# Kernel tuning notes

Measured on AMD Instinct MI355X. Metric: run time of the kernel, lower is better.

## Reference

```python
import jax, jax.numpy as jnp
import numpy as np

N = 50000          # num_assets / nodes
E = 1_600_000      # edges (avg degree 32)
F = 128            # num_features
R = 4              # num_relations
H = 1              # heads
O1, O2 = 15, 10    # RGATConv out_channels (hard-coded in module)
NEG_SLOPE = 0.2    # leaky_relu slope in RGATConv
BN_EPS = 1e-5


def setup_inputs() -> dict:
    key = jax.random.key(0)
    ks = jax.random.split(key, 24)
    s = 0.1
    return {
        "node_emb": jax.random.normal(ks[0], (N, F), jnp.float32),
        "edge_index": jax.random.randint(ks[1], (2, E), 0, N),
        "edge_types": jax.random.randint(ks[2], (E,), 0, R),
        "edge_attr": jax.random.normal(ks[3], (E, 1), jnp.float32),
        # RGATConv layer 1 params
        "W1": jax.random.normal(ks[4], (R, F, H * O1), jnp.float32) * s,
        "q1": jax.random.normal(ks[5], (H * O1, H), jnp.float32) * s,
        "k1": jax.random.normal(ks[6], (H * O1, H), jnp.float32) * s,
        "e1": jax.random.normal(ks[7], (H * O1, H), jnp.float32) * s,
        "We1": jax.random.normal(ks[8], (1, H * O1), jnp.float32) * s,  # lin_edge
        "b1": jax.random.normal(ks[9], (H * O1,), jnp.float32) * s,
        # RGATConv layer 2 params
        "W2": jax.random.normal(ks[10], (R, H * O1, H * O2), jnp.float32) * s,
        "q2": jax.random.normal(ks[11], (H * O2, H), jnp.float32) * s,
        "k2": jax.random.normal(ks[12], (H * O2, H), jnp.float32) * s,
        "e2": jax.random.normal(ks[13], (H * O2, H), jnp.float32) * s,
        "We2": jax.random.normal(ks[14], (1, H * O2), jnp.float32) * s,
        "b2": jax.random.normal(ks[15], (O2,), jnp.float32) * s,
        # BatchNorm affine params
        "g1": 1.0 + jax.random.normal(ks[16], (H * O1,), jnp.float32) * 0.05,
        "beta1": jax.random.normal(ks[17], (H * O1,), jnp.float32) * 0.05,
        "g2": 1.0 + jax.random.normal(ks[18], (O2,), jnp.float32) * 0.05,
        "beta2": jax.random.normal(ks[19], (O2,), jnp.float32) * 0.05,
        # head Linear(10, 1)
        "w_head": jax.random.normal(ks[20], (O2, 1), jnp.float32) * s,
        "b_head": jax.random.normal(ks[21], (1,), jnp.float32) * s,
    }


def _segment_softmax(alpha, dst, n):
    amax = jax.ops.segment_max(alpha, dst, num_segments=n)
    ex = jnp.exp(alpha - amax[dst])
    denom = jax.ops.segment_sum(ex, dst, num_segments=n)
    return ex / (denom[dst] + 1e-16)


def _rgat(x, src, dst, etype, eattr, W, q, k, e, We, b, heads, out_ch, concat):
    n = x.shape[0]
    # per-relation transform of all nodes, then gather per-edge (same math as
    # PyG's per-edge bmm with W[edge_type])
    xt = jnp.einsum('nf,rfo->nro', x, W)            # [N, R, H*O]
    out_i = xt[dst, etype]                          # [E, H*O] (target)
    out_j = xt[src, etype]                          # [E, H*O] (source)
    alpha = out_i @ q + out_j @ k + (eattr @ We) @ e  # [E, H]
    alpha = jax.nn.leaky_relu(alpha, NEG_SLOPE)
    alpha = _segment_softmax(alpha, dst, n)          # across-relation softmax over dst
    msg = (alpha[:, :, None] * out_j.reshape(-1, heads, out_ch)).reshape(-1, heads * out_ch)
    agg = jax.ops.segment_sum(msg, dst, num_segments=n)
    if not concat:
        agg = agg.reshape(n, heads, out_ch).mean(axis=1)
    return agg + b


def _bn_elu(x, g, beta):
    # training-mode BatchNorm1d (batch statistics, biased variance) + ELU
    mu = x.mean(axis=0)
    var = x.var(axis=0)
    xh = (x - mu) / jnp.sqrt(var + BN_EPS)
    return jax.nn.elu(xh * g + beta)


def reference(node_emb, edge_index, edge_types, edge_attr,
              W1, q1, k1, e1, We1, b1,
              W2, q2, k2, e2, We2, b2,
              g1, beta1, g2, beta2, w_head, b_head):
    src, dst = edge_index[0], edge_index[1]
    x = _rgat(node_emb, src, dst, edge_types, edge_attr,
              W1, q1, k1, e1, We1, b1, H, O1, True)
    x = _bn_elu(x, g1, beta1)
    x = _rgat(x, src, dst, edge_types, edge_attr,
              W2, q2, k2, e2, We2, b2, H, O2, False)
    x = _bn_elu(x, g2, beta2)
    return x @ w_head + b_head                       # [N, 1]
```

## Files before the change

kernel.cpp:

```cpp
#include <hip/hip_runtime.h>


typedef unsigned short ushort_t;
typedef unsigned int uint_t;
typedef __attribute__((ext_vector_type(8))) short bf16x8;
typedef __attribute__((ext_vector_type(4))) float f32x4;

#define NEG_SLOPE 0.2f
#define BN_EPS 1e-5f
#define NBUCK 512

__device__ __forceinline__ float bf2f(ushort_t u) {
    return __uint_as_float(((uint_t)u) << 16);
}
__device__ __forceinline__ ushort_t f2bf(float f) {
    uint_t x = __float_as_uint(f);
    x += 0x7FFFu + ((x >> 16) & 1u);
    return (ushort_t)(x >> 16);
}
__device__ __forceinline__ float h2f(ushort_t u) {
    _Float16 h = __builtin_bit_cast(_Float16, u);
    return (float)h;
}
__device__ __forceinline__ ushort_t f2h(float f) {
    _Float16 h = (_Float16)f;
    return __builtin_bit_cast(ushort_t, h);
}
__device__ __forceinline__ float loadf(const void* p, int i, int isb) {
    return isb ? bf2f(((const ushort_t*)p)[i]) : ((const float*)p)[i];
}
__device__ __forceinline__ float sel4(float a0, float a1, float a2, float a3, int et) {
    float lo = (et == 1) ? a1 : a0;
    float hi = (et == 3) ? a3 : a2;
    return (et >= 2) ? hi : lo;
}

__global__ __launch_bounds__(256) void k_prep(const uint_t* __restrict__ x,
                                              const void* __restrict__ W1,
                                              const void* __restrict__ W2,
                                              const void* __restrict__ q1b,
                                              const void* __restrict__ k1b,
                                              const void* __restrict__ We1,
                                              const void* __restrict__ e1v,
                                              const void* __restrict__ We2,
                                              const void* __restrict__ e2v,
                                              int* __restrict__ dflag,
                                              int* __restrict__ bcur,
                                              float* __restrict__ stats1,
                                              float* __restrict__ stats2,
                                              float* __restrict__ cbuf,
                                              ushort_t* __restrict__ Wsw,
                                              float* __restrict__ Wf2, int cap) {
    __shared__ int cnt;
    int t = threadIdx.x;
    if (t == 0) cnt = 0;
    __syncthreads();
    uint_t u = x[t * 37];
    uint_t lo_exp = (u >> 7) & 0xFF;
    atomicAdd(&cnt, (lo_exp >= 96 && lo_exp <= 150) ? 1 : 0);
    __syncthreads();
    int isb = (cnt > 192) ? 1 : 0;
    if (blockIdx.x == 0) {
        if (t == 0) {
            dflag[0] = isb;
            float c1 = 0.f;
            for (int o = 0; o < 15; ++o) c1 += loadf(We1, o, isb) * loadf(e1v, o, isb);
            float c2 = 0.f;
            for (int o = 0; o < 10; ++o) c2 += loadf(We2, o, isb) * loadf(e2v, o, isb);
            cbuf[0] = c1;
            cbuf[1] = c2;
        }
        for (int i = t; i < NBUCK; i += 256) bcur[i] = i * cap;
        stats1[t] = 0.f;
        stats2[t] = 0.f;
        for (int idx = t; idx < 15 * 40; idx += 256) {
            int f = idx / 40, j = idx % 40, r = j / 10, o = j % 10;
            Wf2[idx] = loadf(W2, (r * 15 + f) * 10 + o, isb);
        }
    }
    for (int idx = blockIdx.x * 256 + t; idx < 20 * 64 * 8; idx += gridDim.x * 256) {
        int j = idx & 7, lane = (idx >> 3) & 63, fr = idx >> 9;
        int ks = fr / 5, ct = fr % 5;
        int k = ks * 32 + (lane >> 4) * 8 + j;
        int c = ct * 16 + (lane & 15);
        float v = 0.f;
        if (c < 64) {
            int r = c >> 4, o = c & 15;
            if (o < 15) {
                v = loadf(W1, (r * 128 + k) * 15 + o, isb);
            } else {
                float s = 0.f;
#pragma unroll
                for (int oo = 0; oo < 15; ++oo)
                    s += loadf(W1, (r * 128 + k) * 15 + oo, isb) * loadf(k1b, oo, isb);
                v = s;
            }
        } else if (c < 68) {
            int r = c - 64;
            float s = 0.f;
#pragma unroll
            for (int oo = 0; oo < 15; ++oo)
                s += loadf(W1, (r * 128 + k) * 15 + oo, isb) * loadf(q1b, oo, isb);
            v = s;
        }
        Wsw[idx] = f2bf(v);
    }
}

__global__ __launch_bounds__(512) void k_bucket(const int* __restrict__ ei,
                                                const int* __restrict__ et,
                                                const void* __restrict__ ea,
                                                const int* __restrict__ flag,
                                                int* __restrict__ bcur,
                                                int2* __restrict__ tmp,
                                                int E, int npb) {
    extern __shared__ int2 srec[];
    __shared__ int cnt[NBUCK];
    __shared__ int lofs[NBUCK + 1];
    __shared__ int gpos[NBUCK];
    int t = threadIdx.x;
    int isb = flag[0];
    cnt[t] = 0;
    __syncthreads();
    int e0 = blockIdx.x * 8192;
    for (int i = 0; i < 16; ++i) {
        int e = e0 + i * 512 + t;
        if (e < E) atomicAdd(&cnt[ei[E + e] / npb], 1);
    }
    __syncthreads();
    int myc = cnt[t];
    for (int off = 1; off < NBUCK; off <<= 1) {
        int v = (t >= off) ? cnt[t - off] : 0;
        __syncthreads();
        cnt[t] += v;
        __syncthreads();
    }
    lofs[t] = cnt[t] - myc;
    if (t == NBUCK - 1) lofs[NBUCK] = cnt[NBUCK - 1];
    __syncthreads();
    cnt[t] = lofs[t];
    __syncthreads();
    for (int i = 0; i < 16; ++i) {
        int e = e0 + i * 512 + t;
        if (e < E) {
            int d = ei[E + e];
            int b = d / npb;
            int ldst = d - b * npb;
            int idx = atomicAdd(&cnt[b], 1);
            int2 r;
            r.x = (int)((uint_t)ei[e] | ((uint_t)et[e] << 23) | ((uint_t)ldst << 25));
            r.y = __float_as_int(loadf(ea, e, isb));
            srec[idx] = r;
        }
    }
    __syncthreads();
    int c_b = lofs[t + 1] - lofs[t];
    gpos[t] = atomicAdd(&bcur[t], c_b);
    __syncthreads();
    int total = lofs[NBUCK];
    for (int i = t; i < total; i += 512) {
        int lo = 0, hi = NBUCK - 1;
        while (lo < hi) {
            int mid = (lo + hi + 1) >> 1;
            if (lofs[mid] <= i) lo = mid; else hi = mid - 1;
        }
        tmp[gpos[lo] + (i - lofs[lo])] = srec[i];
    }
}

__global__ __launch_bounds__(256) void k_b2csr(const int2* __restrict__ tmp,
                                               const int* __restrict__ bcur,
                                               int* __restrict__ rs,
                                               int* __restrict__ re,
                                               int2* __restrict__ ebuf,
                                               int N, int npb, int cap) {
    __shared__ int cnt[128];
    __shared__ int lofs[129];
    int b = blockIdx.x, t = threadIdx.x;
    int s0 = b * cap;
    int s1 = bcur[b];
    if (t < 128) cnt[t] = 0;
    __syncthreads();
    for (int p = s0 + t; p < s1; p += 256) {
        uint_t x = (uint_t)tmp[p].x;
        atomicAdd(&cnt[(x >> 25) & 0x7F], 1);
    }
    __syncthreads();
    int myc = (t < 128) ? cnt[t] : 0;
    for (int off = 1; off < 128; off <<= 1) {
        int v = (t >= off && t < 128) ? cnt[t - off] : 0;
        __syncthreads();
        if (t < 128) cnt[t] += v;
        __syncthreads();
    }
    if (t < 128) {
        lofs[t] = cnt[t] - myc;
        if (t == 127) lofs[128] = cnt[127];
    }
    __syncthreads();
    int node0 = b * npb;
    if (t < npb && node0 + t < N) {
        rs[node0 + t] = s0 + lofs[t];
        re[node0 + t] = s0 + lofs[t + 1];
    }
    if (t < 128) cnt[t] = lofs[t];
    __syncthreads();
    for (int p = s0 + t; p < s1; p += 256) {
        int2 r = tmp[p];
        uint_t x = (uint_t)r.x;
        int ldst = (x >> 25) & 0x7F;
        int idx = atomicAdd(&cnt[ldst], 1);
        int2 o;
        o.x = (int)(x & 0x7FFFFF) | (((int)(x >> 23) & 3) << 20);
        o.y = (int)(((uint_t)(node0 + ldst) << 16) |
                    (uint_t)f2bf(__int_as_float(r.y)));
        ebuf[s0 + idx] = o;
    }
}

__global__ __launch_bounds__(256) void k_t1(const void* __restrict__ xin,
                                            const ushort_t* __restrict__ Wsw,
                                            const int* __restrict__ flag,
                                            ushort_t* __restrict__ xt,
                                            float* __restrict__ dq,
                                            int N, int ntiles, int nwaves) {
    int isb = flag[0];
    int lane = threadIdx.x & 63;
    int gw = blockIdx.x * 4 + (threadIdx.x >> 6);
    bf16x8 bfr[20];
    const uint4* wq = (const uint4*)Wsw;
#pragma unroll
    for (int fr = 0; fr < 20; ++fr)
        bfr[fr] = __builtin_bit_cast(bf16x8, wq[fr * 64 + lane]);
    int row = lane & 15, quad = lane >> 4;
    for (int tile = gw; tile < ntiles; tile += nwaves) {
        int n0 = tile * 16;
        f32x4 acc[5];
#pragma unroll
        for (int ct = 0; ct < 5; ++ct) acc[ct] = (f32x4){0.f, 0.f, 0.f, 0.f};
        int nA = n0 + row;
        if (nA >= N) nA = N - 1;
#pragma unroll
        for (int ks = 0; ks < 4; ++ks) {
            bf16x8 af;
            if (isb) {
                uint4 u = *(const uint4*)((const ushort_t*)xin + (size_t)nA * 128 + ks * 32 + quad * 8);
                af = __builtin_bit_cast(bf16x8, u);
            } else {
                const float* xf = (const float*)xin + (size_t)nA * 128 + ks * 32 + quad * 8;
#pragma unroll
                for (int j = 0; j < 8; ++j) af[j] = (short)f2bf(xf[j]);
            }
#pragma unroll
            for (int ct = 0; ct < 5; ++ct)
                acc[ct] = __builtin_amdgcn_mfma_f32_16x16x32_bf16(af, bfr[ks * 5 + ct], acc[ct], 0, 0, 0);
        }
#pragma unroll
        for (int i = 0; i < 4; ++i) {
            int n = n0 + quad * 4 + i;
            if (n < N) {
#pragma unroll
                for (int ct = 0; ct < 4; ++ct) {
                    float val = acc[ct][i];
                    ushort_t bits = (row == 15) ? f2h(val) : f2bf(val);
                    xt[(size_t)n * 64 + ct * 16 + row] = bits;
                }
                if (row < 4) dq[n * 4 + row] = acc[4][i];
            }
        }
    }
}

__global__ __launch_bounds__(256) void k_t2(const float* __restrict__ in,
                                            const float* __restrict__ stats,
                                            const void* __restrict__ g,
                                            const void* __restrict__ beta,
                                            const float* __restrict__ Wf,
                                            const void* __restrict__ qb,
                                            const void* __restrict__ kb,
                                            const int* __restrict__ flag,
                                            ushort_t* __restrict__ xt,
                                            float* __restrict__ dq, int N) {
    int isb = flag[0];
    int t = threadIdx.x;
    int lane = t & 63;
    int r = t >> 6;
    int n = blockIdx.x * 64 + lane;
    if (n >= N) return;
    float invN = 1.f / (float)N;
    float v[15];
#pragma unroll
    for (int c = 0; c < 15; ++c) {
        float mean = stats[c * 16] * invN;
        float var = stats[c * 16 + 8] * invN - mean * mean;
        float inv = rsqrtf(var + BN_EPS);
        float h = (in[(size_t)n * 15 + c] - mean) * inv * loadf(g, c, isb) + loadf(beta, c, isb);
        v[c] = h > 0.f ? h : expm1f(h);
    }
    float acc[10];
#pragma unroll
    for (int o = 0; o < 10; ++o) acc[o] = 0.f;
#pragma unroll
    for (int f = 0; f < 15; ++f) {
        const float* wp = Wf + f * 40 + r * 10;
#pragma unroll
        for (int o = 0; o < 10; ++o) acc[o] += v[f] * wp[o];
    }
    float sq = 0.f, sk = 0.f;
#pragma unroll
    for (int o = 0; o < 10; ++o) {
        sq += acc[o] * loadf(qb, o, isb);
        sk += acc[o] * loadf(kb, o, isb);
    }
    dq[n * 4 + r] = sq;
    ushort_t* xr = xt + (size_t)n * 64 + r * 16;
    uint_t pk[8];
#pragma unroll
    for (int j = 0; j < 5; ++j)
        pk[j] = (uint_t)f2bf(acc[2 * j]) | ((uint_t)f2bf(acc[2 * j + 1]) << 16);
    pk[5] = 0; pk[6] = 0;
    pk[7] = ((uint_t)f2h(sk)) << 16;
    *(uint4*)(xr)     = make_uint4(pk[0], pk[1], pk[2], pk[3]);
    *(uint4*)(xr + 8) = make_uint4(pk[4], pk[5], pk[6], pk[7]);
}

template <int O>
__global__ __launch_bounds__(256) void k_gather(const int* __restrict__ rs,
                                                const int* __restrict__ re,
                                                const int2* __restrict__ ebuf,
                                                const ushort_t* __restrict__ xt,
                                                const float* __restrict__ dq,
                                                const float* __restrict__ cp,
                                                const void* __restrict__ bb,
                                                const int* __restrict__ flag,
                                                float* __restrict__ out, int N) {
    int isb = flag[0];
    int lane = threadIdx.x & 63;
    int w = threadIdx.x >> 6;
    int n = blockIdx.x * 4 + w;
    if (n >= N) return;
    int start = rs[n], end = re[n];
    int ch = lane & 15;
    int gb = lane & 48;
    bool hi15 = (ch == 15);
    float c = cp[0];
    float q0 = dq[n * 4], q1 = dq[n * 4 + 1], q2 = dq[n * 4 + 2], q3 = dq[n * 4 + 3];
    float acc = 0.f, s = 0.f;
    int p = start + (gb >> 4);
    for (; p + 12 < end; p += 16) {
        int2 v0 = ebuf[p];
        int2 v1 = ebuf[p + 4];
        int2 v2 = ebuf[p + 8];
        int2 v3 = ebuf[p + 12];
        ushort_t u0 = xt[(size_t)((v0.x & 0xFFFFF) * 4 + (v0.x >> 20)) * 16 + ch];
        ushort_t u1 = xt[(size_t)((v1.x & 0xFFFFF) * 4 + (v1.x >> 20)) * 16 + ch];
        ushort_t u2 = xt[(size_t)((v2.x & 0xFFFFF) * 4 + (v2.x >> 20)) * 16 + ch];
        ushort_t u3 = xt[(size_t)((v3.x & 0xFFFFF) * 4 + (v3.x >> 20)) * 16 + ch];
        float x0 = hi15 ? h2f(u0) : bf2f(u0);
        float x1 = hi15 ? h2f(u1) : bf2f(u1);
        float x2 = hi15 ? h2f(u2) : bf2f(u2);
        float x3 = hi15 ? h2f(u3) : bf2f(u3);
        float dk0 = __shfl(x0, gb + 15, 64);
        float dk1 = __shfl(x1, gb + 15, 64);
        float dk2 = __shfl(x2, gb + 15, 64);
        float dk3 = __shfl(x3, gb + 15, 64);
        float a0 = sel4(q0, q1, q2, q3, v0.x >> 20) + dk0 + c * bf2f((ushort_t)(v0.y & 0xFFFFu));
        float a1 = sel4(q0, q1, q2, q3, v1.x >> 20) + dk1 + c * bf2f((ushort_t)(v1.y & 0xFFFFu));
        float a2 = sel4(q0, q1, q2, q3, v2.x >> 20) + dk2 + c * bf2f((ushort_t)(v2.y & 0xFFFFu));
        float a3 = sel4(q0, q1, q2, q3, v3.x >> 20) + dk3 + c * bf2f((ushort_t)(v3.y & 0xFFFFu));
        float e0 = __expf(fmaxf(a0, NEG_SLOPE * a0));
        float e1 = __expf(fmaxf(a1, NEG_SLOPE * a1));
        float e2 = __expf(fmaxf(a2, NEG_SLOPE * a2));
        float e3 = __expf(fmaxf(a3, NEG_SLOPE * a3));
        s += (e0 + e1) + (e2 + e3);
        acc += e0 * x0;
        acc += e1 * x1;
        acc += e2 * x2;
        acc += e3 * x3;
    }
    for (; p < end; p += 4) {
        int2 v = ebuf[p];
        ushort_t u = xt[(size_t)((v.x & 0xFFFFF) * 4 + (v.x >> 20)) * 16 + ch];
        float x = hi15 ? h2f(u) : bf2f(u);
        float dk = __shfl(x, gb + 15, 64);
        float a = sel4(q0, q1, q2, q3, v.x >> 20) + dk + c * bf2f((ushort_t)(v.y & 0xFFFFu));
        float e = __expf(fmaxf(a, NEG_SLOPE * a));
        acc += e * x;
        s += e;
    }
    s   += __shfl_xor(s, 16, 64);
    s   += __shfl_xor(s, 32, 64);
    acc += __shfl_xor(acc, 16, 64);
    acc += __shfl_xor(acc, 32, 64);
    if (lane < O) out[(size_t)n * O + lane] = acc / (s + 1e-16f) + loadf(bb, lane, isb);
}

template <int C>
__global__ __launch_bounds__(256) void k_bnstats(const float* __restrict__ in,
                                                 float* __restrict__ S, int N) {
    int t = threadIdx.x;
    int ch = t & 15, rg = t >> 4;
    float s1 = 0.f, s2 = 0.f;
    int row0 = blockIdx.x * 256;
    int rowEnd = row0 + 256;
    if (rowEnd > N) rowEnd = N;
    if (ch < C) {
        for (int r = row0 + rg; r < rowEnd; r += 16) {
            float v = in[(size_t)r * C + ch];
            s1 += v;
            s2 += v * v;
        }
    }
    __shared__ float L1[256], L2[256];
    L1[t] = s1; L2[t] = s2;
    __syncthreads();
    for (int k = 128; k >= 16; k >>= 1) {
        if (t < k) { L1[t] += L1[t + k]; L2[t] += L2[t + k]; }
        __syncthreads();
    }
    if (t < C) {
        atomicAdd(&S[t * 16], L1[t]);
        atomicAdd(&S[t * 16 + 8], L2[t]);
    }
}

__global__ __launch_bounds__(256) void k_head(const float* __restrict__ in,
                                              const float* __restrict__ stats,
                                              const void* __restrict__ g,
                                              const void* __restrict__ beta,
                                              const void* __restrict__ wh,
                                              const void* __restrict__ bh,
                                              const int* __restrict__ flag,
                                              void* __restrict__ out, int N) {
    int isb = flag[0];
    int n = blockIdx.x * 256 + threadIdx.x;
    if (n >= N) return;
    float invN = 1.f / (float)N;
    float r = loadf(bh, 0, isb);
#pragma unroll
    for (int c = 0; c < 10; ++c) {
        float mean = stats[c * 16] * invN;
        float var = stats[c * 16 + 8] * invN - mean * mean;
        float inv = rsqrtf(var + BN_EPS);
        float h = (in[(size_t)n * 10 + c] - mean) * inv * loadf(g, c, isb) + loadf(beta, c, isb);
        float e = h > 0.f ? h : expm1f(h);
        r += e * loadf(wh, c, isb);
    }
    if (isb) ((ushort_t*)out)[n] = f2bf(r);
    else     ((float*)out)[n] = r;
}

extern "C" void kernel_launch(void* const* d_in, const int* in_sizes, int n_in,
                              void* d_out, int out_size, void* d_ws, size_t ws_size,
                              hipStream_t stream) {
    const void* node_emb  = d_in[0];
    const int*  edge_index = (const int*)d_in[1];
    const int*  edge_types = (const int*)d_in[2];
    const void* edge_attr = d_in[3];
    const void* W1  = d_in[4];
    const void* q1  = d_in[5];
    const void* k1  = d_in[6];
    const void* e1  = d_in[7];
    const void* We1 = d_in[8];
    const void* b1  = d_in[9];
    const void* W2  = d_in[10];
    const void* q2  = d_in[11];
    const void* k2  = d_in[12];
    const void* e2  = d_in[13];
    const void* We2 = d_in[14];
    const void* b2  = d_in[15];
    const void* g1  = d_in[16];
    const void* beta1 = d_in[17];
    const void* g2  = d_in[18];
    const void* beta2 = d_in[19];
    const void* w_head = d_in[20];
    const void* b_head = d_in[21];

    int N = in_sizes[0] / 128;
    int E = in_sizes[1] / 2;
    int npb = (N + NBUCK - 1) / NBUCK;
    int nbuck = (N + npb - 1) / npb;
    int cap = E / nbuck + 512;
    size_t slots = (size_t)nbuck * cap;

    char* ws = (char*)d_ws;
    size_t off = 0;
    auto alloc = [&](size_t bytes) -> void* {
        void* p = ws + off;
        off = (off + bytes + 255) & ~(size_t)255;
        return p;
    };
    int*   rs      = (int*)alloc((size_t)N * 4);
    int*   re      = (int*)alloc((size_t)N * 4);
    int*   bcur    = (int*)alloc((NBUCK) * 4);
    int*   dflag   = (int*)alloc(256);
    float* cbuf    = (float*)alloc(256);
    int2*  ebuf    = (int2*)alloc(slots * 8);
    size_t big = (size_t)N * 64 * 2;
    if (slots * 8 > big) big = slots * 8;
    ushort_t* xt1  = (ushort_t*)alloc(big);
    int2*  etmp    = (int2*)xt1;
    float* dq1     = (float*)alloc((size_t)N * 16);
    float* out1    = (float*)alloc((size_t)N * 15 * 4);
    float* stats1  = (float*)alloc(256 * 4);
    float* stats2  = (float*)alloc(256 * 4);
    ushort_t* Wsw  = (ushort_t*)alloc(20 * 64 * 8 * 2);
    float* Wf2     = (float*)alloc(600 * 4);
    ushort_t* xt2 = xt1;
    float* dq2  = dq1;
    float* out2 = out1;

    int NB_N = (N + 255) / 256;
    int NB_T2 = (N + 63) / 64;
    int NB_G = (N + 3) / 4;
    int NB_B = (E + 8191) / 8192;
    int ntiles = (N + 15) / 16;
    int NB_T1 = 391;
    int nwaves = NB_T1 * 4;

    k_prep<<<40, 256, 0, stream>>>((const uint_t*)node_emb, W1, W2, q1, k1,
                                   We1, e1, We2, e2,
                                   dflag, bcur, stats1, stats2, cbuf, Wsw, Wf2, cap);
    k_bucket<<<NB_B, 512, 8192 * sizeof(int2), stream>>>(edge_index, edge_types, edge_attr,
                                                         dflag, bcur, etmp, E, npb);
    k_b2csr<<<nbuck, 256, 0, stream>>>(etmp, bcur, rs, re, ebuf, N, npb, cap);

    k_t1<<<NB_T1, 256, 0, stream>>>(node_emb, Wsw, dflag, xt1, dq1, N, ntiles, nwaves);
    k_gather<15><<<NB_G, 256, 0, stream>>>(rs, re, ebuf, xt1, dq1, cbuf, b1, dflag, out1, N);
    k_bnstats<15><<<NB_N, 256, 0, stream>>>(out1, stats1, N);
    k_t2<<<NB_T2, 256, 0, stream>>>(out1, stats1, g1, beta1, Wf2, q2, k2, dflag, xt2, dq2, N);
    k_gather<10><<<NB_G, 256, 0, stream>>>(rs, re, ebuf, xt2, dq2, cbuf + 1, b2, dflag, out2, N);
    k_bnstats<10><<<NB_N, 256, 0, stream>>>(out2, stats2, N);
    k_head<<<NB_N, 256, 0, stream>>>(out2, stats2, g2, beta2, w_head, b_head, dflag, d_out, N);
}
```

Before: 317.9 us.

## Replace two-level bucketed CSR build with global histogram, scan, atomic scatter

Replaces the shared-memory bucket sort plus per-bucket CSR pass with a straightforward CSR build: a global atomic degree histogram, a per-block prefix scan (each block re-sums all preceding degrees), and a scatter that places each edge using per-node global atomic cursors. This removes the intermediate tmp buffer pass and the heavy shared-memory sorting. In exchange it relies on 1.6M scattered global atomics twice, loses the locality of the old scatter writes, and the scan repeatedly rereads deg, which costs quadratic work across blocks. Edge order within each node becomes nondeterministic.

Measured after the change: 473.7 us. +49.0%, slower.

```diff
diff --git a/kernel.cpp b/kernel.cpp
--- a/kernel.cpp
+++ b/kernel.cpp
@@ -8,7 +8,6 @@
 
 #define NEG_SLOPE 0.2f
 #define BN_EPS 1e-5f
-#define NBUCK 512
 
 __device__ __forceinline__ float bf2f(ushort_t u) {
     return __uint_as_float(((uint_t)u) << 16);
@@ -45,12 +44,12 @@
                                               const void* __restrict__ We2,
                                               const void* __restrict__ e2v,
                                               int* __restrict__ dflag,
-                                              int* __restrict__ bcur,
+                                              int* __restrict__ deg,
                                               float* __restrict__ stats1,
                                               float* __restrict__ stats2,
                                               float* __restrict__ cbuf,
                                               ushort_t* __restrict__ Wsw,
-                                              float* __restrict__ Wf2, int cap) {
+                                              float* __restrict__ Wf2, int N) {
     __shared__ int cnt;
     int t = threadIdx.x;
     if (t == 0) cnt = 0;
@@ -60,6 +59,7 @@
     atomicAdd(&cnt, (lo_exp >= 96 && lo_exp <= 150) ? 1 : 0);
     __syncthreads();
     int isb = (cnt > 192) ? 1 : 0;
+    for (int i = blockIdx.x * 256 + t; i < N; i += gridDim.x * 256) deg[i] = 0;
     if (blockIdx.x == 0) {
         if (t == 0) {
             dflag[0] = isb;
@@ -70,7 +70,6 @@
             cbuf[0] = c1;
             cbuf[1] = c2;
         }
-        for (int i = t; i < NBUCK; i += 256) bcur[i] = i * cap;
         stats1[t] = 0.f;
         stats2[t] = 0.f;
         for (int idx = t; idx < 15 * 40; idx += 256) {
@@ -107,114 +106,61 @@
     }
 }
 
-__global__ __launch_bounds__(512) void k_bucket(const int* __restrict__ ei,
-                                                const int* __restrict__ et,
-                                                const void* __restrict__ ea,
-                                                const int* __restrict__ flag,
-                                                int* __restrict__ bcur,
-                                                int2* __restrict__ tmp,
-                                                int E, int npb) {
-    extern __shared__ int2 srec[];
-    __shared__ int cnt[NBUCK];
-    __shared__ int lofs[NBUCK + 1];
-    __shared__ int gpos[NBUCK];
-    int t = threadIdx.x;
+__global__ __launch_bounds__(256) void k_hist(const int* __restrict__ ei,
+                                              int* __restrict__ deg, int E) {
+    for (int e = blockIdx.x * 256 + threadIdx.x; e < E; e += gridDim.x * 256)
+        atomicAdd(&deg[ei[E + e]], 1);
+}
+
+__global__ __launch_bounds__(256) void k_scan(const int* __restrict__ deg,
+                                              int* __restrict__ rs,
+                                              int* __restrict__ re,
+                                              int* __restrict__ cur, int N) {
+    __shared__ int L[256];
+    int b = blockIdx.x, t = threadIdx.x;
+    int base = b * 256;
+    int s = 0;
+    for (int i = t; i < base; i += 256) s += deg[i];
+    L[t] = s;
+    __syncthreads();
+    for (int k = 128; k; k >>= 1) {
+        if (t < k) L[t] += L[t + k];
+        __syncthreads();
+    }
+    int off = L[0];
+    __syncthreads();
+    int n = base + t;
+    int d = (n < N) ? deg[n] : 0;
+    L[t] = d;
+    __syncthreads();
+    for (int o = 1; o < 256; o <<= 1) {
+        int v = (t >= o) ? L[t - o] : 0;
+        __syncthreads();
+        L[t] += v;
+        __syncthreads();
+    }
+    if (n < N) {
+        int r0 = off + L[t] - d;
+        rs[n] = r0;
+        re[n] = r0 + d;
+        cur[n] = r0;
+    }
+}
+
+__global__ __launch_bounds__(256) void k_scatter(const int* __restrict__ ei,
+                                                 const int* __restrict__ et,
+                                                 const void* __restrict__ ea,
+                                                 const int* __restrict__ flag,
+                                                 int* __restrict__ cur,
+                                                 int2* __restrict__ ebuf, int E) {
     int isb = flag[0];
-    cnt[t] = 0;
-    __syncthreads();
-    int e0 = blockIdx.x * 8192;
-    for (int i = 0; i < 16; ++i) {
-        int e = e0 + i * 512 + t;
-        if (e < E) atomicAdd(&cnt[ei[E + e] / npb], 1);
-    }
-    __syncthreads();
-    int myc = cnt[t];
-    for (int off = 1; off < NBUCK; off <<= 1) {
-        int v = (t >= off) ? cnt[t - off] : 0;
-        __syncthreads();
-        cnt[t] += v;
-        __syncthreads();
-    }
-    lofs[t] = cnt[t] - myc;
-    if (t == NBUCK - 1) lofs[NBUCK] = cnt[NBUCK - 1];
-    __syncthreads();
-    cnt[t] = lofs[t];
-    __syncthreads();
-    for (int i = 0; i < 16; ++i) {
-        int e = e0 + i * 512 + t;
-        if (e < E) {
-            int d = ei[E + e];
-            int b = d / npb;
-            int ldst = d - b * npb;
-            int idx = atomicAdd(&cnt[b], 1);
-            int2 r;
-            r.x = (int)((uint_t)ei[e] | ((uint_t)et[e] << 23) | ((uint_t)ldst << 25));
-            r.y = __float_as_int(loadf(ea, e, isb));
-            srec[idx] = r;
-        }
-    }
-    __syncthreads();
-    int c_b = lofs[t + 1] - lofs[t];
-    gpos[t] = atomicAdd(&bcur[t], c_b);
-    __syncthreads();
-    int total = lofs[NBUCK];
-    for (int i = t; i < total; i += 512) {
-        int lo = 0, hi = NBUCK - 1;
-        while (lo < hi) {
-            int mid = (lo + hi + 1) >> 1;
-            if (lofs[mid] <= i) lo = mid; else hi = mid - 1;
-        }
-        tmp[gpos[lo] + (i - lofs[lo])] = srec[i];
-    }
-}
-
-__global__ __launch_bounds__(256) void k_b2csr(const int2* __restrict__ tmp,
-                                               const int* __restrict__ bcur,
-                                               int* __restrict__ rs,
-                                               int* __restrict__ re,
-                                               int2* __restrict__ ebuf,
-                                               int N, int npb, int cap) {
-    __shared__ int cnt[128];
-    __shared__ int lofs[129];
-    int b = blockIdx.x, t = threadIdx.x;
-    int s0 = b * cap;
-    int s1 = bcur[b];
-    if (t < 128) cnt[t] = 0;
-    __syncthreads();
-    for (int p = s0 + t; p < s1; p += 256) {
-        uint_t x = (uint_t)tmp[p].x;
-        atomicAdd(&cnt[(x >> 25) & 0x7F], 1);
-    }
-    __syncthreads();
-    int myc = (t < 128) ? cnt[t] : 0;
-    for (int off = 1; off < 128; off <<= 1) {
-        int v = (t >= off && t < 128) ? cnt[t - off] : 0;
-        __syncthreads();
-        if (t < 128) cnt[t] += v;
-        __syncthreads();
-    }
-    if (t < 128) {
-        lofs[t] = cnt[t] - myc;
-        if (t == 127) lofs[128] = cnt[127];
-    }
-    __syncthreads();
-    int node0 = b * npb;
-    if (t < npb && node0 + t < N) {
-        rs[node0 + t] = s0 + lofs[t];
-        re[node0 + t] = s0 + lofs[t + 1];
-    }
-    if (t < 128) cnt[t] = lofs[t];
-    __syncthreads();
-    for (int p = s0 + t; p < s1; p += 256) {
-        int2 r = tmp[p];
-        uint_t x = (uint_t)r.x;
-        int ldst = (x >> 25) & 0x7F;
-        int idx = atomicAdd(&cnt[ldst], 1);
+    for (int e = blockIdx.x * 256 + threadIdx.x; e < E; e += gridDim.x * 256) {
+        int d = ei[E + e];
+        int idx = atomicAdd(&cur[d], 1);
         int2 o;
-        o.x = (int)(x & 0x7FFFFF) | (((int)(x >> 23) & 3) << 20);
-        o.y = (int)(((uint_t)(node0 + ldst) << 16) |
-                    (uint_t)f2bf(__int_as_float(r.y)));
-        ebuf[s0 + idx] = o;
+        o.x = ei[e] | (et[e] << 20);
+        o.y = (int)(((uint_t)d << 16) | (uint_t)f2bf(loadf(ea, e, isb)));
+        ebuf[idx] = o;
     }
 }
 
@@ -478,10 +424,6 @@
 
     int N = in_sizes[0] / 128;
     int E = in_sizes[1] / 2;
-    int npb = (N + NBUCK - 1) / NBUCK;
-    int nbuck = (N + npb - 1) / npb;
-    int cap = E / nbuck + 512;
-    size_t slots = (size_t)nbuck * cap;
 
     char* ws = (char*)d_ws;
     size_t off = 0;
@@ -492,14 +434,12 @@
     };
     int*   rs      = (int*)alloc((size_t)N * 4);
     int*   re      = (int*)alloc((size_t)N * 4);
-    int*   bcur    = (int*)alloc((NBUCK) * 4);
+    int*   cur     = (int*)alloc((size_t)N * 4);
+    int*   deg     = (int*)alloc((size_t)N * 4);
     int*   dflag   = (int*)alloc(256);
     float* cbuf    = (float*)alloc(256);
-    int2*  ebuf    = (int2*)alloc(slots * 8);
-    size_t big = (size_t)N * 64 * 2;
-    if (slots * 8 > big) big = slots * 8;
-    ushort_t* xt1  = (ushort_t*)alloc(big);
-    int2*  etmp    = (int2*)xt1;
+    int2*  ebuf    = (int2*)alloc((size_t)E * 8);
+    ushort_t* xt1  = (ushort_t*)alloc((size_t)N * 64 * 2);
     float* dq1     = (float*)alloc((size_t)N * 16);
     float* out1    = (float*)alloc((size_t)N * 15 * 4);
     float* stats1  = (float*)alloc(256 * 4);
@@ -513,17 +453,18 @@
     int NB_N = (N + 255) / 256;
     int NB_T2 = (N + 63) / 64;
     int NB_G = (N + 3) / 4;
-    int NB_B = (E + 8191) / 8192;
+    int NB_E = 2048;
     int ntiles = (N + 15) / 16;
     int NB_T1 = 391;
     int nwaves = NB_T1 * 4;
 
     k_prep<<<40, 256, 0, stream>>>((const uint_t*)node_emb, W1, W2, q1, k1,
                                    We1, e1, We2, e2,
-                                   dflag, bcur, stats1, stats2, cbuf, Wsw, Wf2, cap);
-    k_bucket<<<NB_B, 512, 8192 * sizeof(int2), stream>>>(edge_index, edge_types, edge_attr,
-                                                         dflag, bcur, etmp, E, npb);
-    k_b2csr<<<nbuck, 256, 0, stream>>>(etmp, bcur, rs, re, ebuf, N, npb, cap);
+                                   dflag, deg, stats1, stats2, cbuf, Wsw, Wf2, N);
+    k_hist<<<NB_E, 256, 0, stream>>>(edge_index, deg, E);
+    k_scan<<<NB_N, 256, 0, stream>>>(deg, rs, re, cur, N);
+    k_scatter<<<NB_E, 256, 0, stream>>>(edge_index, edge_types, edge_attr,
+                                        dflag, cur, ebuf, E);
 
     k_t1<<<NB_T1, 256, 0, stream>>>(node_emb, Wsw, dflag, xt1, dq1, N, ntiles, nwaves);
     k_gather<15><<<NB_G, 256, 0, stream>>>(rs, re, ebuf, xt1, dq1, cbuf, b1, dflag, out1, N);
```
